# Optimization experiments

Measured on AMD Instinct MI355X. Metric: run time of the kernel, lower is better.

Reference implementation:

```python
import jax, jax.numpy as jnp
import numpy as np

N = 16384          # total samples (row 0 = anchor)
NPOS = N // 2      # labels: first half == 1 (positives), second half == 0 (negatives)
NNEG = N - NPOS
D = 128            # embedding dim
ALPHA = 0.5
MARGIN = 1.0
TEMPERATURE = 1.0
EPS = 1e-8
SQRT2 = 1.4142135623730951


def setup_inputs() -> dict:
    key = jax.random.key(0)
    k1, k2 = jax.random.split(key)
    est_means = jax.random.normal(k1, (N, D), dtype=jnp.float32)
    # variances must be positive
    est_vars = jax.random.uniform(k2, (N, D), dtype=jnp.float32, minval=0.01, maxval=1.0)
    # deterministic half/half labels so n_pos, n_neg are static (JIT-friendly)
    y_true = jnp.concatenate([jnp.ones((NPOS,), jnp.int32), jnp.zeros((NNEG,), jnp.int32)])
    return {"y_true": y_true, "est_means": est_means, "est_vars": est_vars, "NmulPnN": float(N)}


def reference(y_true, est_means, est_vars, NmulPnN):
    # static-size nonzero (exact counts by construction)
    idx_pos = jnp.nonzero(y_true == 1, size=NPOS)[0]
    idx_neg = jnp.nonzero(y_true == 0, size=NNEG)[0]

    muA = est_means[0]          # [D]
    varA = est_vars[0]          # [D]
    muP = est_means[idx_pos]    # [P, D]
    varP = est_vars[idx_pos]
    muN = est_means[idx_neg]    # [Q, D]
    varN = est_vars[idx_neg]

    muA2 = muA * muA
    muP2 = muP * muP
    muN2 = muN * muN

    # mu[i,j] = sum_d (muP2+varP-2 muA muP)[i,d] - sum_d (muN2+varN-2 muA muN)[j,d]
    sP = jnp.sum(muP2 + varP - 2.0 * muA * muP, axis=1)   # [P]
    sN = jnp.sum(muN2 + varN - 2.0 * muA * muN, axis=1)   # [Q]
    mu = sP[:, None] - sN[None, :]                        # [P, Q]

    # variance terms: T1 depends only on P, T2 only on N, T3 = 4 muP muN varA (cross)
    T1 = (varP * varP + 2.0 * muP2 * varP + 2.0 * (varA + muA2) * (varP + muP2)
          - 2.0 * muA2 * muP2 - 4.0 * muA * muP * varP)
    T2 = (varN * varN + 2.0 * muN2 * varN + 2.0 * (varA + muA2) * (varN + muN2)
          - 2.0 * muA2 * muN2 - 4.0 * muA * muN * varN)
    t1 = jnp.sum(T1, axis=1)                              # [P]
    t2 = jnp.sum(T2, axis=1)                              # [Q]
    cross = jnp.einsum('pd,qd->pq', muP * varA, muN)      # sum_d muP muN varA -> [P, Q]

    sigma2 = 2.0 * t1[:, None] + 2.0 * t2[None, :] - 8.0 * cross
    sigma = jnp.sqrt(jnp.clip(sigma2, 0.0))

    # Normal(mu, sigma+eps).cdf(margin/temperature)
    x = (MARGIN / TEMPERATURE - mu) / (sigma + EPS)
    probs = 0.5 * (1.0 + jax.lax.erf(x / SQRT2))

    loss = -jnp.sum(jnp.log(probs + EPS))
    const_ = NmulPnN / (ALPHA * float(NPOS * NNEG))
    return const_ * loss
```

## Files before the change

### kernel.cpp

```cpp
#include <hip/hip_runtime.h>
#include <hip/hip_bf16.h>
#include <math.h>

#define NTOT 16384
#define NP   8192
#define NQ   8192
#define DIM  128
#define TBLN 4096
#define TBL_SCALE 256.0f
#define INV_SQRT2 0.70710678118654752f

typedef float f32x4 __attribute__((ext_vector_type(4)));
typedef __bf16 bf16x8 __attribute__((ext_vector_type(8)));

__device__ __forceinline__ float wave_reduce_sum(float v) {
#pragma unroll
    for (int off = 32; off > 0; off >>= 1)
        v += __shfl_xor(v, off, 64);
    return v;
}

__global__ __launch_bounds__(256)
void ptl_prep(const float* __restrict__ means,
              const float* __restrict__ vars,
              __hip_bfloat16* __restrict__ pv,
              __hip_bfloat16* __restrict__ nb,
              float2* __restrict__ rowPack,
              float2* __restrict__ colPack,
              float* __restrict__ tblG,
              float* __restrict__ out)
{
    const int wid  = threadIdx.x >> 6;
    const int lane = threadIdx.x & 63;
    const int r    = (blockIdx.x << 2) + wid;
    const int d    = lane << 1;

    if (blockIdx.x == 0 && threadIdx.x == 0) out[0] = 0.f;

    const float2 mu   = *reinterpret_cast<const float2*>(means + (size_t)r * DIM + d);
    const float2 var  = *reinterpret_cast<const float2*>(vars  + (size_t)r * DIM + d);
    const float2 muA  = *reinterpret_cast<const float2*>(means + d);
    const float2 varA = *reinterpret_cast<const float2*>(vars  + d);

    float s = 0.f, t = 0.f;
    {
        const float m = mu.x, v = var.x, ma = muA.x, va = varA.x;
        const float m2 = m * m, ma2 = ma * ma;
        s += m2 + v - 2.f * ma * m;
        t += v * v + 2.f * m2 * v + 2.f * (va + ma2) * (v + m2)
           - 2.f * ma2 * m2 - 4.f * ma * m * v;
    }
    {
        const float m = mu.y, v = var.y, ma = muA.y, va = varA.y;
        const float m2 = m * m, ma2 = ma * ma;
        s += m2 + v - 2.f * ma * m;
        t += v * v + 2.f * m2 * v + 2.f * (va + ma2) * (v + m2)
           - 2.f * ma2 * m2 - 4.f * ma * m * v;
    }
    s = wave_reduce_sum(s);
    t = wave_reduce_sum(t);

    if (r < NP) {
        __hip_bfloat162 pb;
        pb.x = __float2bfloat16(mu.x * varA.x);
        pb.y = __float2bfloat16(mu.y * varA.y);
        *reinterpret_cast<__hip_bfloat162*>(pv + (size_t)r * DIM + d) = pb;
        if (lane == 0) rowPack[r] = make_float2(1.f - s, 2.f * t);
    } else {
        const int q = r - NP;
        __hip_bfloat162 qb;
        qb.x = __float2bfloat16(mu.x);
        qb.y = __float2bfloat16(mu.y);
        *reinterpret_cast<__hip_bfloat162*>(nb + (size_t)q * DIM + d) = qb;
        if (lane == 0) colPack[q] = make_float2(s, 2.f * t);
    }

    if (blockIdx.x < 16) {
        const int k = blockIdx.x * 256 + threadIdx.x;
        const float xc = -8.f + ((float)k + 0.5f) / TBL_SCALE;
        tblG[k] = -logf(0.5f * erfcf(-xc * INV_SQRT2) + 1e-8f);
    }
}

__global__ __launch_bounds__(256, 4)
void ptl_main(const __hip_bfloat16* __restrict__ pv,
              const __hip_bfloat16* __restrict__ nb,
              const float2* __restrict__ rowPack,
              const float2* __restrict__ colPack,
              const float* __restrict__ tblG,
              const float* __restrict__ nmul,
              float* __restrict__ out)
{
    const int wid  = threadIdx.x >> 6;
    const int lane = threadIdx.x & 63;
    const int bi   = blockIdx.x >> 6;
    const int bj   = blockIdx.x & 63;
    const int wr   = wid >> 1, wc = wid & 1;
    const int i0   = bi * 128 + wr * 64;
    const int j0   = bj * 128 + wc * 64;
    const int l16  = lane & 15;
    const int l4   = lane >> 4;

    __shared__ float tbl[2 * TBLN];
    {
        const float4* g4 = (const float4*)tblG;
        float4* l4p = (float4*)tbl;
#pragma unroll
        for (int t = threadIdx.x; t < TBLN / 4; t += 256) {
            const float4 v = g4[t];
            l4p[t] = v;
            l4p[t + TBLN / 4] = v;
        }
    }
    __syncthreads();

    f32x4 acc[4][4];
#pragma unroll
    for (int m = 0; m < 4; ++m)
#pragma unroll
        for (int n = 0; n < 4; ++n)
            acc[m][n] = (f32x4){0.f, 0.f, 0.f, 0.f};

    const __hip_bfloat16* Ab = pv + (size_t)(i0 + l16) * DIM + l4 * 8;
    const __hip_bfloat16* Bb = nb + (size_t)(j0 + l16) * DIM + l4 * 8;

#pragma unroll
    for (int kq = 0; kq < 4; ++kq) {
        bf16x8 a[4], b[4];
#pragma unroll
        for (int m = 0; m < 4; ++m)
            a[m] = *reinterpret_cast<const bf16x8*>(Ab + m * 16 * DIM + kq * 32);
#pragma unroll
        for (int n = 0; n < 4; ++n)
            b[n] = *reinterpret_cast<const bf16x8*>(Bb + n * 16 * DIM + kq * 32);
#pragma unroll
        for (int m = 0; m < 4; ++m)
#pragma unroll
            for (int n = 0; n < 4; ++n)
                acc[m][n] = __builtin_amdgcn_mfma_f32_16x16x32_bf16(a[m], b[n], acc[m][n], 0, 0, 0);
    }

    float2 cp[4];
#pragma unroll
    for (int n = 0; n < 4; ++n)
        cp[n] = colPack[j0 + n * 16 + l16];

    const unsigned laneSel = ((unsigned)lane & 1u) << 12;

    float lacc0 = 0.f, lacc1 = 0.f, lacc2 = 0.f, lacc3 = 0.f;
#pragma unroll
    for (int m = 0; m < 4; ++m) {
        float2 rp[4];
#pragma unroll
        for (int rr = 0; rr < 4; ++rr)
            rp[rr] = rowPack[i0 + m * 16 + l4 * 4 + rr];

        float us[16];
#pragma unroll
        for (int n = 0; n < 4; ++n) {
#pragma unroll
            for (int rr = 0; rr < 4; ++rr) {
                const float c   = acc[m][n][rr];
                const float t12 = rp[rr].y + cp[n].y;
                const float omm = rp[rr].x + cp[n].x;
                float s2 = fmaf(-8.f, c, t12);
                s2 = fmaxf(s2, 1e-20f);
                const float x = omm * __builtin_amdgcn_rsqf(s2);
                float u = fmaf(x, TBL_SCALE, 2048.0f);
                us[n * 4 + rr] = __builtin_amdgcn_fmed3f(u, 0.0f, 4095.99f);
            }
        }

        float pk[16];
#pragma unroll
        for (int e = 0; e < 16; ++e)
            pk[e] = tbl[(unsigned)us[e] + laneSel];

#pragma unroll
        for (int e = 0; e < 16; e += 4) {
            lacc0 += pk[e];
            lacc1 += pk[e + 1];
            lacc2 += pk[e + 2];
            lacc3 += pk[e + 3];
        }
    }

    float lsum = (lacc0 + lacc1) + (lacc2 + lacc3);
    lsum = wave_reduce_sum(lsum);

    __shared__ float wsum[4];
    if (lane == 0) wsum[wid] = lsum;
    __syncthreads();
    if (threadIdx.x == 0) {
        const float bsum = (wsum[0] + wsum[1]) + (wsum[2] + wsum[3]);
        const float cst = nmul[0] / (0.5f * (float)NP * (float)NQ);
        atomicAdd(out, cst * bsum);
    }
}

extern "C" void kernel_launch(void* const* d_in, const int* in_sizes, int n_in,
                              void* d_out, int out_size, void* d_ws, size_t ws_size,
                              hipStream_t stream)
{
    const float* means = (const float*)d_in[1];
    const float* vars  = (const float*)d_in[2];
    const float* nmul  = (const float*)d_in[3];
    float* out = (float*)d_out;

    __hip_bfloat16* pv = (__hip_bfloat16*)d_ws;
    __hip_bfloat16* nb = pv + (size_t)NP * DIM;
    float2* rowPack = (float2*)((char*)d_ws + (size_t)(NP + NQ) * DIM * sizeof(__hip_bfloat16));
    float2* colPack = rowPack + NP;
    float* tblG     = (float*)(colPack + NQ);

    ptl_prep<<<NTOT / 4, 256, 0, stream>>>(means, vars, pv, nb, rowPack, colPack, tblG, out);
    ptl_main<<<(NP / 128) * (NQ / 128), 256, 0, stream>>>(pv, nb, rowPack, colPack, tblG, nmul, out);
}
```

Baseline: 149.8 us.

## Replace LDS lookup table with per-lane register table via ds_bpermute and interpolation

Drops the 4096-entry shared-memory table of -log(Phi(x)) and the copy into LDS with its barrier. Each lane now computes one cell of a 64-entry table (value plus bf16 slope) and keeps it in a register. Lookups become ds_bpermute with linear interpolation. Row and column pack values are also loaded once per lane and broadcast through bpermute instead of repeated global loads. This frees LDS and removes the table-load phase, at the cost of a coarser, interpolated approximation over a narrower range (-6.5 to 4.3) and extra ALU work.

After: 163.6 us. +9.2%, slower.

```diff
diff --git a/kernel.cpp b/kernel.cpp
--- a/kernel.cpp
+++ b/kernel.cpp
@@ -6,8 +6,9 @@
 #define NP   8192
 #define NQ   8192
 #define DIM  128
-#define TBLN 4096
-#define TBL_SCALE 256.0f
+#define TLO   -6.5f
+#define CELL  0.16875f
+#define INV_CELL 5.925925926f
 #define INV_SQRT2 0.70710678118654752f
 
 typedef float f32x4 __attribute__((ext_vector_type(4)));
@@ -18,6 +19,12 @@
     for (int off = 32; off > 0; off >>= 1)
         v += __shfl_xor(v, off, 64);
     return v;
+}
+
+__device__ __forceinline__ unsigned f32_to_bf16_rne(float f) {
+    unsigned u = __float_as_uint(f);
+    u += 0x7FFFu + ((u >> 16) & 1u);
+    return u >> 16;
 }
 
 __global__ __launch_bounds__(256)
@@ -27,7 +34,6 @@
               __hip_bfloat16* __restrict__ nb,
               float2* __restrict__ rowPack,
               float2* __restrict__ colPack,
-              float* __restrict__ tblG,
               float* __restrict__ out)
 {
     const int wid  = threadIdx.x >> 6;
@@ -74,12 +80,6 @@
         *reinterpret_cast<__hip_bfloat162*>(nb + (size_t)q * DIM + d) = qb;
         if (lane == 0) colPack[q] = make_float2(s, 2.f * t);
     }
-
-    if (blockIdx.x < 16) {
-        const int k = blockIdx.x * 256 + threadIdx.x;
-        const float xc = -8.f + ((float)k + 0.5f) / TBL_SCALE;
-        tblG[k] = -logf(0.5f * erfcf(-xc * INV_SQRT2) + 1e-8f);
-    }
 }
 
 __global__ __launch_bounds__(256, 4)
@@ -87,7 +87,6 @@
               const __hip_bfloat16* __restrict__ nb,
               const float2* __restrict__ rowPack,
               const float2* __restrict__ colPack,
-              const float* __restrict__ tblG,
               const float* __restrict__ nmul,
               float* __restrict__ out)
 {
@@ -101,18 +100,15 @@
     const int l16  = lane & 15;
     const int l4   = lane >> 4;
 
-    __shared__ float tbl[2 * TBLN];
-    {
-        const float4* g4 = (const float4*)tblG;
-        float4* l4p = (float4*)tbl;
-#pragma unroll
-        for (int t = threadIdx.x; t < TBLN / 4; t += 256) {
-            const float4 v = g4[t];
-            l4p[t] = v;
-            l4p[t + TBLN / 4] = v;
-        }
-    }
-    __syncthreads();
+    const float xlo = TLO + (float)lane * CELL;
+    const float ga  = -logf(0.5f * erfcf(-xlo * INV_SQRT2) + 1e-8f);
+    const float gb  = -logf(0.5f * erfcf(-(xlo + CELL) * INV_SQRT2) + 1e-8f);
+    const int tblpk = (int)((f32_to_bf16_rne(gb - ga) << 16) | f32_to_bf16_rne(ga));
+
+    const float2 rpl = rowPack[i0 + lane];
+    const float2 cpl = colPack[j0 + lane];
+    const int rpx = __float_as_int(rpl.x), rpy = __float_as_int(rpl.y);
+    const int cpx = __float_as_int(cpl.x), cpy = __float_as_int(cpl.y);
 
     f32x4 acc[4][4];
 #pragma unroll
@@ -140,20 +136,24 @@
                 acc[m][n] = __builtin_amdgcn_mfma_f32_16x16x32_bf16(a[m], b[n], acc[m][n], 0, 0, 0);
     }
 
-    float2 cp[4];
-#pragma unroll
-    for (int n = 0; n < 4; ++n)
-        cp[n] = colPack[j0 + n * 16 + l16];
-
-    const unsigned laneSel = ((unsigned)lane & 1u) << 12;
+    float cpx_[4], cpy_[4];
+#pragma unroll
+    for (int n = 0; n < 4; ++n) {
+        const int idx = (n * 16 + l16) << 2;
+        cpx_[n] = __int_as_float(__builtin_amdgcn_ds_bpermute(idx, cpx));
+        cpy_[n] = __int_as_float(__builtin_amdgcn_ds_bpermute(idx, cpy));
+    }
 
     float lacc0 = 0.f, lacc1 = 0.f, lacc2 = 0.f, lacc3 = 0.f;
 #pragma unroll
     for (int m = 0; m < 4; ++m) {
-        float2 rp[4];
-#pragma unroll
-        for (int rr = 0; rr < 4; ++rr)
-            rp[rr] = rowPack[i0 + m * 16 + l4 * 4 + rr];
+        float rpx_[4], rpy_[4];
+#pragma unroll
+        for (int rr = 0; rr < 4; ++rr) {
+            const int idx = (m * 16 + l4 * 4 + rr) << 2;
+            rpx_[rr] = __int_as_float(__builtin_amdgcn_ds_bpermute(idx, rpx));
+            rpy_[rr] = __int_as_float(__builtin_amdgcn_ds_bpermute(idx, rpy));
+        }
 
         float us[16];
 #pragma unroll
@@ -161,27 +161,31 @@
 #pragma unroll
             for (int rr = 0; rr < 4; ++rr) {
                 const float c   = acc[m][n][rr];
-                const float t12 = rp[rr].y + cp[n].y;
-                const float omm = rp[rr].x + cp[n].x;
+                const float t12 = rpy_[rr] + cpy_[n];
+                const float omm = rpx_[rr] + cpx_[n];
                 float s2 = fmaf(-8.f, c, t12);
                 s2 = fmaxf(s2, 1e-20f);
                 const float x = omm * __builtin_amdgcn_rsqf(s2);
-                float u = fmaf(x, TBL_SCALE, 2048.0f);
-                us[n * 4 + rr] = __builtin_amdgcn_fmed3f(u, 0.0f, 4095.99f);
+                float u = fmaf(x, INV_CELL, 38.5185185f);
+                us[n * 4 + rr] = __builtin_amdgcn_fmed3f(u, 0.0f, 63.99f);
             }
         }
 
-        float pk[16];
+        int pk[16];
 #pragma unroll
         for (int e = 0; e < 16; ++e)
-            pk[e] = tbl[(unsigned)us[e] + laneSel];
-
-#pragma unroll
-        for (int e = 0; e < 16; e += 4) {
-            lacc0 += pk[e];
-            lacc1 += pk[e + 1];
-            lacc2 += pk[e + 2];
-            lacc3 += pk[e + 3];
+            pk[e] = __builtin_amdgcn_ds_bpermute(((int)us[e]) << 2, tblpk);
+
+#pragma unroll
+        for (int e = 0; e < 16; ++e) {
+            const float fr = us[e] - (float)((int)us[e]);
+            const float g  = __int_as_float(pk[e] << 16);
+            const float dg = __int_as_float(pk[e] & 0xFFFF0000);
+            const float val = fmaf(fr, dg, g);
+            if ((e & 3) == 0) lacc0 += val;
+            else if ((e & 3) == 1) lacc1 += val;
+            else if ((e & 3) == 2) lacc2 += val;
+            else lacc3 += val;
         }
     }
 
@@ -211,8 +215,7 @@
     __hip_bfloat16* nb = pv + (size_t)NP * DIM;
     float2* rowPack = (float2*)((char*)d_ws + (size_t)(NP + NQ) * DIM * sizeof(__hip_bfloat16));
     float2* colPack = rowPack + NP;
-    float* tblG     = (float*)(colPack + NQ);
-
-    ptl_prep<<<NTOT / 4, 256, 0, stream>>>(means, vars, pv, nb, rowPack, colPack, tblG, out);
-    ptl_main<<<(NP / 128) * (NQ / 128), 256, 0, stream>>>(pv, nb, rowPack, colPack, tblG, nmul, out);
-}
+
+    ptl_prep<<<NTOT / 4, 256, 0, stream>>>(means, vars, pv, nb, rowPack, colPack, out);
+    ptl_main<<<(NP / 128) * (NQ / 128), 256, 0, stream>>>(pv, nb, rowPack, colPack, nmul, out);
+}
```
